# Optimization experiments

Measured on AMD Instinct MI355X. Metric: run time of the kernel, lower is better.

The kernel has to match this reference:

```python
import jax, jax.numpy as jnp
import numpy as np

N, D, E = 100000, 64, 1250000  # nodes, feature dim, total signed edges
H = D // 2                     # per-polarity hidden dim


def _mean_agg(x, src, dst, n):
    """Mean-aggregate messages x[src] at dst over n segments (gather->scatter)."""
    s = jax.ops.segment_sum(x[src], dst, num_segments=n)
    cnt = jax.ops.segment_sum(jnp.ones((src.shape[0], 1), x.dtype), dst, num_segments=n)
    return s / jnp.maximum(cnt, 1.0)


def _lin_w(k, fi, fo):
    b = 1.0 / np.sqrt(fi)
    return jax.random.uniform(k, (fi, fo), jnp.float32, -b, b)


def setup_inputs() -> dict:
    key = jax.random.key(0)
    ks = list(jax.random.split(key, 24))
    init_emb = jax.random.normal(ks[0], (N, D), dtype=jnp.float32)
    src = jax.random.randint(ks[1], (E,), 0, N)
    dst = jax.random.randint(ks[2], (E,), 0, N)
    sign = jnp.where(jax.random.uniform(ks[3], (E,)) < 0.5, 1, -1)
    edge_index_s = jnp.stack([src, dst, sign], axis=1)
    return dict(
        init_emb=init_emb,
        edge_index_s=edge_index_s,
        # conv1 (first_aggr=True): lin([mean_agg, x]) per polarity -> H
        Wp1=_lin_w(ks[4], 2 * D, H), bp1=jnp.zeros((H,), jnp.float32),
        Wn1=_lin_w(ks[5], 2 * D, H), bn1=jnp.zeros((H,), jnp.float32),
        # rest conv: lin([agg_pos, agg_neg, x_half]) per polarity -> H
        Wp2=_lin_w(ks[6], 3 * H, H), bp2=jnp.zeros((H,), jnp.float32),
        Wn2=_lin_w(ks[7], 3 * H, H), bn2=jnp.zeros((H,), jnp.float32),
        # final linear D->D
        Ww=_lin_w(ks[8], D, D), bw=jnp.zeros((D,), jnp.float32),
        # MLP readout: Linear+BN+ReLU, Linear+BN+ReLU, Linear->1 (inference mode)
        Wm1=_lin_w(ks[9], D, D), bm1=jnp.zeros((D,), jnp.float32),
        g1=jnp.ones((D,), jnp.float32), be1=jnp.zeros((D,), jnp.float32),
        rm1=jnp.zeros((D,), jnp.float32), rv1=jnp.ones((D,), jnp.float32),
        Wm2=_lin_w(ks[10], D, D), bm2=jnp.zeros((D,), jnp.float32),
        g2=jnp.ones((D,), jnp.float32), be2=jnp.zeros((D,), jnp.float32),
        rm2=jnp.zeros((D,), jnp.float32), rv2=jnp.ones((D,), jnp.float32),
        Wm3=_lin_w(ks[11], D, 1), bm3=jnp.zeros((1,), jnp.float32),
    )


def reference(init_emb, edge_index_s, Wp1, bp1, Wn1, bn1, Wp2, bp2, Wn2, bn2,
              Ww, bw, Wm1, bm1, g1, be1, rm1, rv1, Wm2, bm2, g2, be2, rm2, rv2,
              Wm3, bm3):
    # split signed edge list into pos / neg edge indices (eager boolean mask,
    # mirrors edge_index_s[edge_index_s[:,2]>0][:, :2].t())
    sign = edge_index_s[:, 2]
    pos = edge_index_s[sign > 0]
    neg = edge_index_s[sign < 0]
    ps, pd = pos[:, 0], pos[:, 1]
    ns, nd = neg[:, 0], neg[:, 1]

    x = init_emb
    # --- first signed conv (first_aggr=True) ---
    ap = _mean_agg(x, ps, pd, N)
    an = _mean_agg(x, ns, nd, N)
    hp = jnp.concatenate([ap, x], -1) @ Wp1 + bp1
    hn = jnp.concatenate([an, x], -1) @ Wn1 + bn1
    z = jnp.tanh(jnp.concatenate([hp, hn], -1))  # [N, D]

    # --- rest signed conv (balance-theory cross-polarity aggregation) ---
    xp, xn = z[:, :H], z[:, H:]
    hp = jnp.concatenate([_mean_agg(xp, ps, pd, N), _mean_agg(xn, ns, nd, N), xp], -1) @ Wp2 + bp2
    hn = jnp.concatenate([_mean_agg(xn, ps, pd, N), _mean_agg(xp, ns, nd, N), xn], -1) @ Wn2 + bn2
    z = jnp.tanh(jnp.concatenate([hp, hn], -1))  # [N, D]

    # --- final linear + tanh ---
    z = jnp.tanh(z @ Ww + bw)

    # --- MLP readout (inference: BN uses running stats, dropout disabled) ---
    def bn(h, g, b, rm, rv):
        return (h - rm) * jax.lax.rsqrt(rv + 1e-5) * g + b

    h = jax.nn.relu(bn(z @ Wm1 + bm1, g1, be1, rm1, rv1))
    h = jax.nn.relu(bn(h @ Wm2 + bm2, g2, be2, rm2, rv2))
    prob = jax.nn.sigmoid(h @ Wm3 + bm3)  # [N, 1]
    return z, prob
```

## Files before the change

kernel.cpp:

```cpp
#include <hip/hip_runtime.h>
#include <hip/hip_bf16.h>

#define CAP 32

typedef __attribute__((ext_vector_type(8))) short bf16x8;
typedef __attribute__((ext_vector_type(4))) float f32x4;

#define MFMA(a, b, c) __builtin_amdgcn_mfma_f32_16x16x32_bf16(a, b, c, 0, 0, 0)

__device__ __forceinline__ unsigned short bf16rn(float f) {
    unsigned u = __builtin_bit_cast(unsigned, f);
    u += 0x7fffu + ((u >> 16) & 1u);
    return (unsigned short)(u >> 16);
}

__device__ __forceinline__ float bf16lo(unsigned u) {
    return __builtin_bit_cast(float, u << 16);
}
__device__ __forceinline__ float bf16hi(unsigned u) {
    return __builtin_bit_cast(float, u & 0xffff0000u);
}
__device__ __forceinline__ unsigned pack2(float a, float b) {
    return (unsigned)bf16rn(a) | ((unsigned)bf16rn(b) << 16);
}

__device__ __forceinline__ bf16x8 packbf8(const float* p) {
    bf16x8 r;
    #pragma unroll
    for (int j = 0; j < 8; ++j) r[j] = (short)bf16rn(p[j]);
    return r;
}

__device__ __forceinline__ bf16x8 wfrag(const float* __restrict__ W, int NN,
                                        int kt, int ct, int q, int c) {
    const float* base = W + (kt * 32 + q * 8) * NN + ct * 16 + c;
    float t[8];
    #pragma unroll
    for (int j = 0; j < 8; ++j) t[j] = base[j * NN];
    return packbf8(t);
}

__device__ __forceinline__ bf16x8 afrag_bf16(const __hip_bfloat16* row, int cw, int q) {
    return *(const bf16x8*)((const short*)row + cw + q * 8);
}

__global__ __launch_bounds__(256) void pg_build_cast(
    const int* __restrict__ ei,
    int* __restrict__ plist, int* __restrict__ nlist,
    int* __restrict__ pcur, int* __restrict__ ncur, int E, int buildBlocks,
    const float* __restrict__ x, __hip_bfloat16* __restrict__ xb, int nx)
{
    int b = blockIdx.x;
    if (b >= buildBlocks) {
        int i = ((b - buildBlocks) * 256 + threadIdx.x) * 4;
        if (i < nx) {
            float4 v = *(const float4*)(x + i);
            ushort4 o;
            o.x = bf16rn(v.x); o.y = bf16rn(v.y);
            o.z = bf16rn(v.z); o.w = bf16rn(v.w);
            *(ushort4*)((unsigned short*)xb + i) = o;
        }
        return;
    }
    int e0 = (b * 256 + threadIdx.x) * 4;
    int s[4], d[4], sg[4];
    bool ok[4];
    #pragma unroll
    for (int k = 0; k < 4; ++k) {
        int e = e0 + k;
        ok[k] = (e < E);
        int ee = ok[k] ? e : 0;
        s[k]  = ei[3 * ee + 0];
        d[k]  = ei[3 * ee + 1];
        sg[k] = ei[3 * ee + 2];
    }
    int slot[4];
    int* dstl[4];
    #pragma unroll
    for (int k = 0; k < 4; ++k) {
        int* cur = (sg[k] > 0) ? pcur : ncur;
        dstl[k]  = ((sg[k] > 0) ? plist : nlist) + (size_t)d[k] * CAP;
        slot[k]  = ok[k] ? atomicAdd(cur + d[k], 1) : CAP;
    }
    #pragma unroll
    for (int k = 0; k < 4; ++k)
        if (slot[k] < CAP) dstl[k][slot[k]] = s[k];
}

__global__ __launch_bounds__(256, 6) void pg_gather(
    const __hip_bfloat16* __restrict__ src,
    const int* __restrict__ plist, const int* __restrict__ nlist,
    const int* __restrict__ pcur, const int* __restrict__ ncur,
    __hip_bfloat16* __restrict__ agg, int N)
{
    int tid = threadIdx.x;
    int w = tid >> 6, lane = tid & 63;
    int grp = lane >> 4;
    int q   = lane & 15;

    #pragma unroll 1
    for (int g = 0; g < 4; ++g) {
        int i0 = blockIdx.x * 64 + w * 16 + g * 4;
        int pd[4], nd[4], pde[4], nde[4], pl[4], nl[4];
        #pragma unroll
        for (int n = 0; n < 4; ++n) {
            int i = min(i0 + n, N - 1);
            pd[n] = __builtin_amdgcn_readfirstlane(pcur[i]);
            nd[n] = __builtin_amdgcn_readfirstlane(ncur[i]);
            pde[n] = min(pd[n], CAP);
            nde[n] = min(nd[n], CAP);
            pl[n] = plist[(size_t)i * CAP + (lane & 31)];
            nl[n] = nlist[(size_t)i * CAP + (lane & 31)];
        }
        int maxd = 0;
        #pragma unroll
        for (int n = 0; n < 4; ++n) maxd = max(maxd, max(pde[n], nde[n]));

        float ps[4][4], ns[4][4];
        #pragma unroll
        for (int n = 0; n < 4; ++n)
            #pragma unroll
            for (int r = 0; r < 4; ++r) { ps[n][r] = 0.f; ns[n][r] = 0.f; }

        #pragma unroll 1
        for (int e = 0; e < maxd; e += 4) {
            #pragma unroll
            for (int n = 0; n < 4; ++n) {
                int p0 = __builtin_amdgcn_readlane(pl[n], (e + 0) < pde[n] ? e + 0 : 0);
                int p1 = __builtin_amdgcn_readlane(pl[n], (e + 1) < pde[n] ? e + 1 : 0);
                int p2 = __builtin_amdgcn_readlane(pl[n], (e + 2) < pde[n] ? e + 2 : 0);
                int p3 = __builtin_amdgcn_readlane(pl[n], (e + 3) < pde[n] ? e + 3 : 0);
                int m0 = __builtin_amdgcn_readlane(nl[n], (e + 0) < nde[n] ? e + 0 : 0);
                int m1 = __builtin_amdgcn_readlane(nl[n], (e + 1) < nde[n] ? e + 1 : 0);
                int m2 = __builtin_amdgcn_readlane(nl[n], (e + 2) < nde[n] ? e + 2 : 0);
                int m3 = __builtin_amdgcn_readlane(nl[n], (e + 3) < nde[n] ? e + 3 : 0);
                unsigned sp = (unsigned)(grp == 0 ? p0 : grp == 1 ? p1 : grp == 2 ? p2 : p3);
                unsigned sn = (unsigned)(grp == 0 ? m0 : grp == 1 ? m1 : grp == 2 ? m2 : m3);
                sp = sp < (unsigned)N ? sp : 0u;
                sn = sn < (unsigned)N ? sn : 0u;
                uint2 pv = *((const uint2*)(src + ((size_t)sp << 6)) + q);
                uint2 nv = *((const uint2*)(src + ((size_t)sn << 6)) + q);
                float wp  = (e + grp < pde[n]) ? 1.f : 0.f;
                float wn_ = (e + grp < nde[n]) ? 1.f : 0.f;
                ps[n][0] = fmaf(wp, bf16lo(pv.x), ps[n][0]);
                ps[n][1] = fmaf(wp, bf16hi(pv.x), ps[n][1]);
                ps[n][2] = fmaf(wp, bf16lo(pv.y), ps[n][2]);
                ps[n][3] = fmaf(wp, bf16hi(pv.y), ps[n][3]);
                ns[n][0] = fmaf(wn_, bf16lo(nv.x), ns[n][0]);
                ns[n][1] = fmaf(wn_, bf16hi(nv.x), ns[n][1]);
                ns[n][2] = fmaf(wn_, bf16lo(nv.y), ns[n][2]);
                ns[n][3] = fmaf(wn_, bf16hi(nv.y), ns[n][3]);
            }
        }
        #pragma unroll
        for (int n = 0; n < 4; ++n) {
            #pragma unroll
            for (int r = 0; r < 4; ++r) {
                ps[n][r] += __shfl_xor(ps[n][r], 16);
                ps[n][r] += __shfl_xor(ps[n][r], 32);
                ns[n][r] += __shfl_xor(ns[n][r], 16);
                ns[n][r] += __shfl_xor(ns[n][r], 32);
            }
            int i = i0 + n;
            if (i < N) {
                float invp = 1.f / fmaxf((float)pd[n], 1.f);
                float invn = 1.f / fmaxf((float)nd[n], 1.f);
                uint2* arow = (uint2*)(agg + ((size_t)i << 7));
                if (grp == 0) {
                    uint2 ow;
                    ow.x = pack2(ps[n][0] * invp, ps[n][1] * invp);
                    ow.y = pack2(ps[n][2] * invp, ps[n][3] * invp);
                    arow[q] = ow;
                } else if (grp == 1) {
                    uint2 ow;
                    ow.x = pack2(ns[n][0] * invn, ns[n][1] * invn);
                    ow.y = pack2(ns[n][2] * invn, ns[n][3] * invn);
                    arow[16 + q] = ow;
                }
            }
        }
    }
}

__global__ __launch_bounds__(256, 3) void pg_gemm1(
    const __hip_bfloat16* __restrict__ xb, const __hip_bfloat16* __restrict__ agg,
    const float* __restrict__ Wp, const float* __restrict__ bp,
    const float* __restrict__ Wn, const float* __restrict__ bn,
    __hip_bfloat16* __restrict__ z1b, int N, int nwv)
{
    int tid = threadIdx.x;
    int w = tid >> 6, lane = tid & 63;
    int q = lane >> 4, c = lane & 15;

    bf16x8 B[2][4][2];
    #pragma unroll
    for (int kt = 0; kt < 4; ++kt)
        #pragma unroll
        for (int ct = 0; ct < 2; ++ct) {
            B[0][kt][ct] = wfrag(Wp, 32, kt, ct, q, c);
            B[1][kt][ct] = wfrag(Wn, 32, kt, ct, q, c);
        }
    float bias[2][2];
    #pragma unroll
    for (int ct = 0; ct < 2; ++ct) {
        bias[0][ct] = bp[ct * 16 + c];
        bias[1][ct] = bn[ct * 16 + c];
    }

    int ntiles = (N + 15) >> 4;
    #pragma unroll 1
    for (int t = blockIdx.x * 4 + w; t < ntiles; t += nwv) {
        int i = min(t * 16 + c, N - 1);
        const __hip_bfloat16* arow = agg + ((size_t)i << 7);
        const __hip_bfloat16* xrow = xb + ((size_t)i << 6);
        bf16x8 aA0 = afrag_bf16(arow, 0, q);
        bf16x8 aA1 = afrag_bf16(arow, 32, q);
        bf16x8 aA2 = afrag_bf16(arow, 64, q);
        bf16x8 aA3 = afrag_bf16(arow, 96, q);
        bf16x8 aX0 = afrag_bf16(xrow, 0, q);
        bf16x8 aX1 = afrag_bf16(xrow, 32, q);
        f32x4 acc[2][2];
        #pragma unroll
        for (int ct = 0; ct < 2; ++ct) {
            f32x4 a = {0.f, 0.f, 0.f, 0.f};
            a = MFMA(aA0, B[0][0][ct], a);
            a = MFMA(aA1, B[0][1][ct], a);
            a = MFMA(aX0, B[0][2][ct], a);
            a = MFMA(aX1, B[0][3][ct], a);
            acc[0][ct] = a;
            f32x4 b = {0.f, 0.f, 0.f, 0.f};
            b = MFMA(aA2, B[1][0][ct], b);
            b = MFMA(aA3, B[1][1][ct], b);
            b = MFMA(aX0, B[1][2][ct], b);
            b = MFMA(aX1, B[1][3][ct], b);
            acc[1][ct] = b;
        }
        #pragma unroll
        for (int h = 0; h < 2; ++h)
            #pragma unroll
            for (int ct = 0; ct < 2; ++ct)
                #pragma unroll
                for (int r = 0; r < 4; ++r) {
                    int row = t * 16 + q * 4 + r;
                    if (row < N)
                        z1b[(size_t)row * 64 + h * 32 + ct * 16 + c] =
                            __float2bfloat16(tanhf(acc[h][ct][r] + bias[h][ct]));
                }
    }
}

__global__ __launch_bounds__(256, 3) void pg_gemm2(
    const __hip_bfloat16* __restrict__ z1b, __hip_bfloat16* agg,
    const float* __restrict__ Wp2, const float* __restrict__ bp2,
    const float* __restrict__ Wn2, const float* __restrict__ bn2,
    int N, int nwv)
{
    int tid = threadIdx.x;
    int w = tid >> 6, lane = tid & 63;
    int q = lane >> 4, c = lane & 15;

    bf16x8 B[2][3][2];
    #pragma unroll
    for (int kt = 0; kt < 3; ++kt)
        #pragma unroll
        for (int ct = 0; ct < 2; ++ct) {
            B[0][kt][ct] = wfrag(Wp2, 32, kt, ct, q, c);
            B[1][kt][ct] = wfrag(Wn2, 32, kt, ct, q, c);
        }
    float bias[2][2];
    #pragma unroll
    for (int ct = 0; ct < 2; ++ct) {
        bias[0][ct] = bp2[ct * 16 + c];
        bias[1][ct] = bn2[ct * 16 + c];
    }

    int ntiles = (N + 15) >> 4;
    #pragma unroll 1
    for (int t = blockIdx.x * 4 + w; t < ntiles; t += nwv) {
        int i = min(t * 16 + c, N - 1);
        const __hip_bfloat16* arow = agg + ((size_t)i << 7);
        const __hip_bfloat16* zrow = z1b + ((size_t)i << 6);
        bf16x8 ap0 = afrag_bf16(arow, 0, q);
        bf16x8 ap1 = afrag_bf16(arow, 96, q);
        bf16x8 an0 = afrag_bf16(arow, 32, q);
        bf16x8 an1 = afrag_bf16(arow, 64, q);
        bf16x8 az0 = afrag_bf16(zrow, 0, q);
        bf16x8 az1 = afrag_bf16(zrow, 32, q);
        f32x4 acc[2][2];
        #pragma unroll
        for (int ct = 0; ct < 2; ++ct) {
            f32x4 a = {0.f, 0.f, 0.f, 0.f};
            a = MFMA(ap0, B[0][0][ct], a);
            a = MFMA(ap1, B[0][1][ct], a);
            a = MFMA(az0, B[0][2][ct], a);
            acc[0][ct] = a;
            f32x4 b = {0.f, 0.f, 0.f, 0.f};
            b = MFMA(an0, B[1][0][ct], b);
            b = MFMA(an1, B[1][1][ct], b);
            b = MFMA(az1, B[1][2][ct], b);
            acc[1][ct] = b;
        }
        #pragma unroll
        for (int h = 0; h < 2; ++h)
            #pragma unroll
            for (int ct = 0; ct < 2; ++ct)
                #pragma unroll
                for (int r = 0; r < 4; ++r) {
                    int row = t * 16 + q * 4 + r;
                    if (row < N)
                        agg[(size_t)row * 128 + h * 32 + ct * 16 + c] =
                            __float2bfloat16(tanhf(acc[h][ct][r] + bias[h][ct]));
                }
    }
}

__global__ __launch_bounds__(256, 2) void pg_mlp(
    float* out, const __hip_bfloat16* __restrict__ z2b,
    const float* __restrict__ Ww,  const float* __restrict__ bw,
    const float* __restrict__ Wm1, const float* __restrict__ bm1,
    const float* __restrict__ g1,  const float* __restrict__ be1,
    const float* __restrict__ rm1, const float* __restrict__ rv1,
    const float* __restrict__ Wm2, const float* __restrict__ bm2,
    const float* __restrict__ g2,  const float* __restrict__ be2,
    const float* __restrict__ rm2, const float* __restrict__ rv2,
    const float* __restrict__ Wm3, const float* __restrict__ bm3,
    int N, int nwv)
{
    __shared__ float xpos[4][16][68];
    int tid = threadIdx.x;
    int w = tid >> 6, lane = tid & 63;
    int q = lane >> 4, c = lane & 15;
    float (*lx)[68] = xpos[w];

    bf16x8 Bw[2][4], B1[2][4], B2[2][4];
    #pragma unroll
    for (int kt = 0; kt < 2; ++kt)
        #pragma unroll
        for (int ct = 0; ct < 4; ++ct) {
            Bw[kt][ct] = wfrag(Ww,  64, kt, ct, q, c);
            B1[kt][ct] = wfrag(Wm1, 64, kt, ct, q, c);
            B2[kt][ct] = wfrag(Wm2, 64, kt, ct, q, c);
        }
    float bwv[4], s1[4], o1[4], s2[4], o2[4], w3[4];
    #pragma unroll
    for (int ct = 0; ct < 4; ++ct) {
        int cc = ct * 16 + c;
        bwv[ct] = bw[cc];
        float a = g1[cc] * rsqrtf(rv1[cc] + 1e-5f);
        s1[ct] = a; o1[ct] = (bm1[cc] - rm1[cc]) * a + be1[cc];
        float b = g2[cc] * rsqrtf(rv2[cc] + 1e-5f);
        s2[ct] = b; o2[ct] = (bm2[cc] - rm2[cc]) * b + be2[cc];
        w3[ct] = Wm3[cc];
    }
    float b3 = bm3[0];

    int ntiles = (N + 15) >> 4;
    #pragma unroll 1
    for (int t = blockIdx.x * 4 + w; t < ntiles; t += nwv) {
        int i = min(t * 16 + c, N - 1);
        const __hip_bfloat16* zrow = z2b + ((size_t)i << 7);
        bf16x8 a0 = afrag_bf16(zrow, 0, q);
        bf16x8 a1 = afrag_bf16(zrow, 32, q);
        f32x4 acc[4];

        #pragma unroll
        for (int ct = 0; ct < 4; ++ct) {
            f32x4 a = {0.f, 0.f, 0.f, 0.f};
            a = MFMA(a0, Bw[0][ct], a);
            a = MFMA(a1, Bw[1][ct], a);
            acc[ct] = a;
        }
        #pragma unroll
        for (int ct = 0; ct < 4; ++ct)
            #pragma unroll
            for (int r = 0; r < 4; ++r) {
                int row = t * 16 + q * 4 + r;
                float v = tanhf(acc[ct][r] + bwv[ct]);
                if (row < N) out[(size_t)row * 64 + ct * 16 + c] = v;
                lx[q * 4 + r][ct * 16 + c] = v;
            }
        {
            const float* pr = &lx[c][0];
            float tb[8];
            *(float4*)tb       = *(const float4*)(pr + q * 8);
            *(float4*)(tb + 4) = *(const float4*)(pr + q * 8 + 4);
            a0 = packbf8(tb);
            *(float4*)tb       = *(const float4*)(pr + 32 + q * 8);
            *(float4*)(tb + 4) = *(const float4*)(pr + 32 + q * 8 + 4);
            a1 = packbf8(tb);
        }

        #pragma unroll
        for (int ct = 0; ct < 4; ++ct) {
            f32x4 a = {0.f, 0.f, 0.f, 0.f};
            a = MFMA(a0, B1[0][ct], a);
            a = MFMA(a1, B1[1][ct], a);
            acc[ct] = a;
        }
        #pragma unroll
        for (int ct = 0; ct < 4; ++ct)
            #pragma unroll
            for (int r = 0; r < 4; ++r)
                lx[q * 4 + r][ct * 16 + c] = fmaxf(acc[ct][r] * s1[ct] + o1[ct], 0.f);
        {
            const float* pr = &lx[c][0];
            float tb[8];
            *(float4*)tb       = *(const float4*)(pr + q * 8);
            *(float4*)(tb + 4) = *(const float4*)(pr + q * 8 + 4);
            a0 = packbf8(tb);
            *(float4*)tb       = *(const float4*)(pr + 32 + q * 8);
            *(float4*)(tb + 4) = *(const float4*)(pr + 32 + q * 8 + 4);
            a1 = packbf8(tb);
        }

        #pragma unroll
        for (int ct = 0; ct < 4; ++ct) {
            f32x4 a = {0.f, 0.f, 0.f, 0.f};
            a = MFMA(a0, B2[0][ct], a);
            a = MFMA(a1, B2[1][ct], a);
            acc[ct] = a;
        }
        float tr[4];
        #pragma unroll
        for (int r = 0; r < 4; ++r) {
            float hs = 0.f;
            #pragma unroll
            for (int ct = 0; ct < 4; ++ct) {
                float h2 = fmaxf(acc[ct][r] * s2[ct] + o2[ct], 0.f);
                hs = fmaf(h2, w3[ct], hs);
            }
            tr[r] = hs;
        }
        #pragma unroll
        for (int m = 1; m < 16; m <<= 1)
            #pragma unroll
            for (int r = 0; r < 4; ++r) tr[r] += __shfl_xor(tr[r], m, 16);
        if (c == 0) {
            #pragma unroll
            for (int r = 0; r < 4; ++r) {
                int row = t * 16 + q * 4 + r;
                if (row < N)
                    out[(size_t)N * 64 + row] = 1.f / (1.f + expf(-(tr[r] + b3)));
            }
        }
    }
}

extern "C" void kernel_launch(void* const* d_in, const int* in_sizes, int n_in,
                              void* d_out, int out_size, void* d_ws, size_t ws_size,
                              hipStream_t stream) {
    const float* x   = (const float*)d_in[0];
    const int*   ei  = (const int*)  d_in[1];
    const float* Wp1 = (const float*)d_in[2];
    const float* bp1 = (const float*)d_in[3];
    const float* Wn1 = (const float*)d_in[4];
    const float* bn1 = (const float*)d_in[5];
    const float* Wp2 = (const float*)d_in[6];
    const float* bp2 = (const float*)d_in[7];
    const float* Wn2 = (const float*)d_in[8];
    const float* bn2 = (const float*)d_in[9];
    const float* Ww  = (const float*)d_in[10];
    const float* bw  = (const float*)d_in[11];
    const float* Wm1 = (const float*)d_in[12];
    const float* bm1 = (const float*)d_in[13];
    const float* g1  = (const float*)d_in[14];
    const float* be1 = (const float*)d_in[15];
    const float* rm1 = (const float*)d_in[16];
    const float* rv1 = (const float*)d_in[17];
    const float* Wm2 = (const float*)d_in[18];
    const float* bm2 = (const float*)d_in[19];
    const float* g2  = (const float*)d_in[20];
    const float* be2 = (const float*)d_in[21];
    const float* rm2 = (const float*)d_in[22];
    const float* rv2 = (const float*)d_in[23];
    const float* Wm3 = (const float*)d_in[24];
    const float* bm3 = (const float*)d_in[25];
    float* out = (float*)d_out;

    int N = in_sizes[0] / 64;
    int E = in_sizes[1] / 3;

    int* plist = (int*)d_ws;
    int* nlist = plist + (size_t)N * CAP;
    int* pcur  = nlist + (size_t)N * CAP;
    int* ncur  = pcur + N;
    __hip_bfloat16* agg = (__hip_bfloat16*)(ncur + N);

    __hip_bfloat16* z1b = (__hip_bfloat16*)out;
    __hip_bfloat16* xb  = (__hip_bfloat16*)((char*)d_out + (size_t)N * 128);

    hipMemsetAsync(pcur, 0, 2 * (size_t)N * sizeof(int), stream);

    int buildBlocks = (E + 1023) / 1024;
    int castBlocks  = (N * 64 / 4 + 255) / 256;
    pg_build_cast<<<buildBlocks + castBlocks, 256, 0, stream>>>(
        ei, plist, nlist, pcur, ncur, E, buildBlocks, x, xb, N * 64);

    int nb = (N + 63) / 64;
    const int gb = 512, nwv = gb * 4;
    pg_gather<<<nb, 256, 0, stream>>>(xb, plist, nlist, pcur, ncur, agg, N);
    pg_gemm1<<<gb, 256, 0, stream>>>(xb, agg, Wp1, bp1, Wn1, bn1, z1b, N, nwv);
    pg_gather<<<nb, 256, 0, stream>>>(z1b, plist, nlist, pcur, ncur, agg, N);
    pg_gemm2<<<gb, 256, 0, stream>>>(z1b, agg, Wp2, bp2, Wn2, bn2, N, nwv);
    pg_mlp<<<gb, 256, 0, stream>>>(out, agg, Ww, bw,
                                   Wm1, bm1, g1, be1, rm1, rv1,
                                   Wm2, bm2, g2, be2, rm2, rv2,
                                   Wm3, bm3, N, nwv);
}
```

Baseline: 258.2 us.

## Fuse neighbor gather with per-layer MFMA GEMM via LDS staging

Merges each gather kernel with the following linear+tanh kernel. The mean aggregates for 16 nodes per wave are staged in LDS and fed straight into the MFMA fragments, so the bf16 agg buffer is no longer written to and re-read from global memory, and two launches are dropped. The gather also now predicates each neighbor load on validity instead of loading a dummy row and multiplying by zero. In exchange, weights are reloaded per block and occupancy is set to 4 waves per SIMD with added LDS use.

```diff
diff --git a/kernel.cpp b/kernel.cpp
--- a/kernel.cpp
+++ b/kernel.cpp
@@ -13,7 +13,6 @@
     u += 0x7fffu + ((u >> 16) & 1u);
     return (unsigned short)(u >> 16);
 }
-
 __device__ __forceinline__ float bf16lo(unsigned u) {
     return __builtin_bit_cast(float, u << 16);
 }
@@ -23,7 +22,6 @@
 __device__ __forceinline__ unsigned pack2(float a, float b) {
     return (unsigned)bf16rn(a) | ((unsigned)bf16rn(b) << 16);
 }
-
 __device__ __forceinline__ bf16x8 packbf8(const float* p) {
     bf16x8 r;
     #pragma unroll
@@ -42,6 +40,14 @@
 
 __device__ __forceinline__ bf16x8 afrag_bf16(const __hip_bfloat16* row, int cw, int q) {
     return *(const bf16x8*)((const short*)row + cw + q * 8);
+}
+
+__device__ __forceinline__ bf16x8 lfrag(const short* lrow, int cw, int q8) {
+    const uint2* p = (const uint2*)(lrow + cw + q8 * 8);
+    uint2 lo = p[0], hi = p[1];
+    uint4 u;
+    u.x = lo.x; u.y = lo.y; u.z = hi.x; u.w = hi.y;
+    return __builtin_bit_cast(bf16x8, u);
 }
 
 __global__ __launch_bounds__(256) void pg_build_cast(
@@ -87,118 +93,110 @@
         if (slot[k] < CAP) dstl[k][slot[k]] = s[k];
 }
 
-__global__ __launch_bounds__(256, 6) void pg_gather(
-    const __hip_bfloat16* __restrict__ src,
+
+#define GATHER_16NODES(SRC)                                                     \
+    for (int g = 0; g < 4; ++g) {                                               \
+        int i0 = base + g * 4;                                                  \
+        int pd[4], nd[4], pde[4], nde[4], pl[4], nl[4];                         \
+        _Pragma("unroll")                                                       \
+        for (int n = 0; n < 4; ++n) {                                           \
+            int i = min(i0 + n, N - 1);                                         \
+            pd[n] = __builtin_amdgcn_readfirstlane(pcur[i]);                    \
+            nd[n] = __builtin_amdgcn_readfirstlane(ncur[i]);                    \
+            pde[n] = min(pd[n], CAP);                                           \
+            nde[n] = min(nd[n], CAP);                                           \
+            pl[n] = plist[(size_t)i * CAP + (lane & 31)];                       \
+            nl[n] = nlist[(size_t)i * CAP + (lane & 31)];                       \
+        }                                                                       \
+        int maxd = 0;                                                           \
+        _Pragma("unroll")                                                       \
+        for (int n = 0; n < 4; ++n) maxd = max(maxd, max(pde[n], nde[n]));      \
+        float ps[4][4], ns[4][4];                                               \
+        _Pragma("unroll")                                                       \
+        for (int n = 0; n < 4; ++n)                                             \
+            _Pragma("unroll")                                                   \
+            for (int r = 0; r < 4; ++r) { ps[n][r] = 0.f; ns[n][r] = 0.f; }     \
+        _Pragma("unroll 1")                                                     \
+        for (int e = 0; e < maxd; e += 4) {                                     \
+            _Pragma("unroll")                                                   \
+            for (int n = 0; n < 4; ++n) {                                       \
+                int p0 = __builtin_amdgcn_readlane(pl[n], (e+0) < pde[n] ? e+0 : 0); \
+                int p1 = __builtin_amdgcn_readlane(pl[n], (e+1) < pde[n] ? e+1 : 0); \
+                int p2 = __builtin_amdgcn_readlane(pl[n], (e+2) < pde[n] ? e+2 : 0); \
+                int p3 = __builtin_amdgcn_readlane(pl[n], (e+3) < pde[n] ? e+3 : 0); \
+                int m0 = __builtin_amdgcn_readlane(nl[n], (e+0) < nde[n] ? e+0 : 0); \
+                int m1 = __builtin_amdgcn_readlane(nl[n], (e+1) < nde[n] ? e+1 : 0); \
+                int m2 = __builtin_amdgcn_readlane(nl[n], (e+2) < nde[n] ? e+2 : 0); \
+                int m3 = __builtin_amdgcn_readlane(nl[n], (e+3) < nde[n] ? e+3 : 0); \
+                unsigned sp = (unsigned)(grp == 0 ? p0 : grp == 1 ? p1 : grp == 2 ? p2 : p3); \
+                unsigned sn = (unsigned)(grp == 0 ? m0 : grp == 1 ? m1 : grp == 2 ? m2 : m3); \
+                if (e + grp < pde[n]) {                                         \
+                    sp = sp < (unsigned)N ? sp : 0u;                            \
+                    uint2 pv = *((const uint2*)((SRC) + ((size_t)sp << 6)) + q);\
+                    ps[n][0] += bf16lo(pv.x); ps[n][1] += bf16hi(pv.x);         \
+                    ps[n][2] += bf16lo(pv.y); ps[n][3] += bf16hi(pv.y);         \
+                }                                                               \
+                if (e + grp < nde[n]) {                                         \
+                    sn = sn < (unsigned)N ? sn : 0u;                            \
+                    uint2 nv = *((const uint2*)((SRC) + ((size_t)sn << 6)) + q);\
+                    ns[n][0] += bf16lo(nv.x); ns[n][1] += bf16hi(nv.x);         \
+                    ns[n][2] += bf16lo(nv.y); ns[n][3] += bf16hi(nv.y);         \
+                }                                                               \
+            }                                                                   \
+        }                                                                       \
+        _Pragma("unroll")                                                       \
+        for (int n = 0; n < 4; ++n) {                                           \
+            _Pragma("unroll")                                                   \
+            for (int r = 0; r < 4; ++r) {                                       \
+                ps[n][r] += __shfl_xor(ps[n][r], 16);                           \
+                ps[n][r] += __shfl_xor(ps[n][r], 32);                           \
+                ns[n][r] += __shfl_xor(ns[n][r], 16);                           \
+                ns[n][r] += __shfl_xor(ns[n][r], 32);                           \
+            }                                                                   \
+            float invp = 1.f / fmaxf((float)pd[n], 1.f);                        \
+            float invn = 1.f / fmaxf((float)nd[n], 1.f);                        \
+            short* lrow = &lds[(g * 4 + n) * 132];                              \
+            if (grp == 0) {                                                     \
+                uint2 ow;                                                       \
+                ow.x = pack2(ps[n][0] * invp, ps[n][1] * invp);                 \
+                ow.y = pack2(ps[n][2] * invp, ps[n][3] * invp);                 \
+                *(uint2*)(lrow + 4 * q) = ow;                                   \
+            } else if (grp == 1) {                                              \
+                uint2 ow;                                                       \
+                ow.x = pack2(ns[n][0] * invn, ns[n][1] * invn);                 \
+                ow.y = pack2(ns[n][2] * invn, ns[n][3] * invn);                 \
+                *(uint2*)(lrow + 64 + 4 * q) = ow;                              \
+            }                                                                   \
+        }                                                                       \
+    }
+
+__global__ __launch_bounds__(256, 4) void pg_layer1(
+    const __hip_bfloat16* __restrict__ xb,
     const int* __restrict__ plist, const int* __restrict__ nlist,
     const int* __restrict__ pcur, const int* __restrict__ ncur,
-    __hip_bfloat16* __restrict__ agg, int N)
+    const float* __restrict__ Wp, const float* __restrict__ bp,
+    const float* __restrict__ Wn, const float* __restrict__ bn,
+    __hip_bfloat16* __restrict__ z1b, int N)
 {
+    __shared__ short smem[4][16 * 132];
     int tid = threadIdx.x;
     int w = tid >> 6, lane = tid & 63;
-    int grp = lane >> 4;
-    int q   = lane & 15;
-
-    #pragma unroll 1
-    for (int g = 0; g < 4; ++g) {
-        int i0 = blockIdx.x * 64 + w * 16 + g * 4;
-        int pd[4], nd[4], pde[4], nde[4], pl[4], nl[4];
-        #pragma unroll
-        for (int n = 0; n < 4; ++n) {
-            int i = min(i0 + n, N - 1);
-            pd[n] = __builtin_amdgcn_readfirstlane(pcur[i]);
-            nd[n] = __builtin_amdgcn_readfirstlane(ncur[i]);
-            pde[n] = min(pd[n], CAP);
-            nde[n] = min(nd[n], CAP);
-            pl[n] = plist[(size_t)i * CAP + (lane & 31)];
-            nl[n] = nlist[(size_t)i * CAP + (lane & 31)];
-        }
-        int maxd = 0;
-        #pragma unroll
-        for (int n = 0; n < 4; ++n) maxd = max(maxd, max(pde[n], nde[n]));
-
-        float ps[4][4], ns[4][4];
-        #pragma unroll
-        for (int n = 0; n < 4; ++n)
-            #pragma unroll
-            for (int r = 0; r < 4; ++r) { ps[n][r] = 0.f; ns[n][r] = 0.f; }
-
-        #pragma unroll 1
-        for (int e = 0; e < maxd; e += 4) {
-            #pragma unroll
-            for (int n = 0; n < 4; ++n) {
-                int p0 = __builtin_amdgcn_readlane(pl[n], (e + 0) < pde[n] ? e + 0 : 0);
-                int p1 = __builtin_amdgcn_readlane(pl[n], (e + 1) < pde[n] ? e + 1 : 0);
-                int p2 = __builtin_amdgcn_readlane(pl[n], (e + 2) < pde[n] ? e + 2 : 0);
-                int p3 = __builtin_amdgcn_readlane(pl[n], (e + 3) < pde[n] ? e + 3 : 0);
-                int m0 = __builtin_amdgcn_readlane(nl[n], (e + 0) < nde[n] ? e + 0 : 0);
-                int m1 = __builtin_amdgcn_readlane(nl[n], (e + 1) < nde[n] ? e + 1 : 0);
-                int m2 = __builtin_amdgcn_readlane(nl[n], (e + 2) < nde[n] ? e + 2 : 0);
-                int m3 = __builtin_amdgcn_readlane(nl[n], (e + 3) < nde[n] ? e + 3 : 0);
-                unsigned sp = (unsigned)(grp == 0 ? p0 : grp == 1 ? p1 : grp == 2 ? p2 : p3);
-                unsigned sn = (unsigned)(grp == 0 ? m0 : grp == 1 ? m1 : grp == 2 ? m2 : m3);
-                sp = sp < (unsigned)N ? sp : 0u;
-                sn = sn < (unsigned)N ? sn : 0u;
-                uint2 pv = *((const uint2*)(src + ((size_t)sp << 6)) + q);
-                uint2 nv = *((const uint2*)(src + ((size_t)sn << 6)) + q);
-                float wp  = (e + grp < pde[n]) ? 1.f : 0.f;
-                float wn_ = (e + grp < nde[n]) ? 1.f : 0.f;
-                ps[n][0] = fmaf(wp, bf16lo(pv.x), ps[n][0]);
-                ps[n][1] = fmaf(wp, bf16hi(pv.x), ps[n][1]);
-                ps[n][2] = fmaf(wp, bf16lo(pv.y), ps[n][2]);
-                ps[n][3] = fmaf(wp, bf16hi(pv.y), ps[n][3]);
-                ns[n][0] = fmaf(wn_, bf16lo(nv.x), ns[n][0]);
-                ns[n][1] = fmaf(wn_, bf16hi(nv.x), ns[n][1]);
-                ns[n][2] = fmaf(wn_, bf16lo(nv.y), ns[n][2]);
-                ns[n][3] = fmaf(wn_, bf16hi(nv.y), ns[n][3]);
-            }
-        }
-        #pragma unroll
-        for (int n = 0; n < 4; ++n) {
-            #pragma unroll
-            for (int r = 0; r < 4; ++r) {
-                ps[n][r] += __shfl_xor(ps[n][r], 16);
-                ps[n][r] += __shfl_xor(ps[n][r], 32);
-                ns[n][r] += __shfl_xor(ns[n][r], 16);
-                ns[n][r] += __shfl_xor(ns[n][r], 32);
-            }
-            int i = i0 + n;
-            if (i < N) {
-                float invp = 1.f / fmaxf((float)pd[n], 1.f);
-                float invn = 1.f / fmaxf((float)nd[n], 1.f);
-                uint2* arow = (uint2*)(agg + ((size_t)i << 7));
-                if (grp == 0) {
-                    uint2 ow;
-                    ow.x = pack2(ps[n][0] * invp, ps[n][1] * invp);
-                    ow.y = pack2(ps[n][2] * invp, ps[n][3] * invp);
-                    arow[q] = ow;
-                } else if (grp == 1) {
-                    uint2 ow;
-                    ow.x = pack2(ns[n][0] * invn, ns[n][1] * invn);
-                    ow.y = pack2(ns[n][2] * invn, ns[n][3] * invn);
-                    arow[16 + q] = ow;
-                }
-            }
-        }
-    }
-}
-
-__global__ __launch_bounds__(256, 3) void pg_gemm1(
-    const __hip_bfloat16* __restrict__ xb, const __hip_bfloat16* __restrict__ agg,
-    const float* __restrict__ Wp, const float* __restrict__ bp,
-    const float* __restrict__ Wn, const float* __restrict__ bn,
-    __hip_bfloat16* __restrict__ z1b, int N, int nwv)
-{
-    int tid = threadIdx.x;
-    int w = tid >> 6, lane = tid & 63;
-    int q = lane >> 4, c = lane & 15;
-
+    int grp = lane >> 4, q = lane & 15;
+    short* lds = smem[w];
+    int base = blockIdx.x * 64 + w * 16;
+
+    GATHER_16NODES(xb)
+
+    __builtin_amdgcn_sched_barrier(0);
+
+    int q8 = lane >> 4, c = lane & 15;
     bf16x8 B[2][4][2];
     #pragma unroll
     for (int kt = 0; kt < 4; ++kt)
         #pragma unroll
         for (int ct = 0; ct < 2; ++ct) {
-            B[0][kt][ct] = wfrag(Wp, 32, kt, ct, q, c);
-            B[1][kt][ct] = wfrag(Wn, 32, kt, ct, q, c);
+            B[0][kt][ct] = wfrag(Wp, 32, kt, ct, q8, c);
+            B[1][kt][ct] = wfrag(Wn, 32, kt, ct, q8, c);
         }
     float bias[2][2];
     #pragma unroll
@@ -206,66 +204,71 @@
         bias[0][ct] = bp[ct * 16 + c];
         bias[1][ct] = bn[ct * 16 + c];
     }
-
-    int ntiles = (N + 15) >> 4;
-    #pragma unroll 1
-    for (int t = blockIdx.x * 4 + w; t < ntiles; t += nwv) {
-        int i = min(t * 16 + c, N - 1);
-        const __hip_bfloat16* arow = agg + ((size_t)i << 7);
-        const __hip_bfloat16* xrow = xb + ((size_t)i << 6);
-        bf16x8 aA0 = afrag_bf16(arow, 0, q);
-        bf16x8 aA1 = afrag_bf16(arow, 32, q);
-        bf16x8 aA2 = afrag_bf16(arow, 64, q);
-        bf16x8 aA3 = afrag_bf16(arow, 96, q);
-        bf16x8 aX0 = afrag_bf16(xrow, 0, q);
-        bf16x8 aX1 = afrag_bf16(xrow, 32, q);
-        f32x4 acc[2][2];
-        #pragma unroll
-        for (int ct = 0; ct < 2; ++ct) {
-            f32x4 a = {0.f, 0.f, 0.f, 0.f};
-            a = MFMA(aA0, B[0][0][ct], a);
-            a = MFMA(aA1, B[0][1][ct], a);
-            a = MFMA(aX0, B[0][2][ct], a);
-            a = MFMA(aX1, B[0][3][ct], a);
-            acc[0][ct] = a;
-            f32x4 b = {0.f, 0.f, 0.f, 0.f};
-            b = MFMA(aA2, B[1][0][ct], b);
-            b = MFMA(aA3, B[1][1][ct], b);
-            b = MFMA(aX0, B[1][2][ct], b);
-            b = MFMA(aX1, B[1][3][ct], b);
-            acc[1][ct] = b;
-        }
-        #pragma unroll
-        for (int h = 0; h < 2; ++h)
-            #pragma unroll
-            for (int ct = 0; ct < 2; ++ct)
-                #pragma unroll
-                for (int r = 0; r < 4; ++r) {
-                    int row = t * 16 + q * 4 + r;
-                    if (row < N)
-                        z1b[(size_t)row * 64 + h * 32 + ct * 16 + c] =
-                            __float2bfloat16(tanhf(acc[h][ct][r] + bias[h][ct]));
-                }
-    }
-}
-
-__global__ __launch_bounds__(256, 3) void pg_gemm2(
-    const __hip_bfloat16* __restrict__ z1b, __hip_bfloat16* agg,
+    int i = min(base + c, N - 1);
+    const __hip_bfloat16* xrow = xb + ((size_t)i << 6);
+    const short* lrow = &lds[c * 132];
+    bf16x8 aA0 = lfrag(lrow, 0, q8);
+    bf16x8 aA1 = lfrag(lrow, 32, q8);
+    bf16x8 aA2 = lfrag(lrow, 64, q8);
+    bf16x8 aA3 = lfrag(lrow, 96, q8);
+    bf16x8 aX0 = afrag_bf16(xrow, 0, q8);
+    bf16x8 aX1 = afrag_bf16(xrow, 32, q8);
+    f32x4 acc[2][2];
+    #pragma unroll
+    for (int ct = 0; ct < 2; ++ct) {
+        f32x4 a = {0.f, 0.f, 0.f, 0.f};
+        a = MFMA(aA0, B[0][0][ct], a);
+        a = MFMA(aA1, B[0][1][ct], a);
+        a = MFMA(aX0, B[0][2][ct], a);
+        a = MFMA(aX1, B[0][3][ct], a);
+        acc[0][ct] = a;
+        f32x4 b = {0.f, 0.f, 0.f, 0.f};
+        b = MFMA(aA2, B[1][0][ct], b);
+        b = MFMA(aA3, B[1][1][ct], b);
+        b = MFMA(aX0, B[1][2][ct], b);
+        b = MFMA(aX1, B[1][3][ct], b);
+        acc[1][ct] = b;
+    }
+    #pragma unroll
+    for (int h = 0; h < 2; ++h)
+        #pragma unroll
+        for (int ct = 0; ct < 2; ++ct)
+            #pragma unroll
+            for (int r = 0; r < 4; ++r) {
+                int row = base + q8 * 4 + r;
+                if (row < N)
+                    z1b[(size_t)row * 64 + h * 32 + ct * 16 + c] =
+                        __float2bfloat16(tanhf(acc[h][ct][r] + bias[h][ct]));
+            }
+}
+
+__global__ __launch_bounds__(256, 4) void pg_layer2(
+    const __hip_bfloat16* __restrict__ z1b,
+    const int* __restrict__ plist, const int* __restrict__ nlist,
+    const int* __restrict__ pcur, const int* __restrict__ ncur,
     const float* __restrict__ Wp2, const float* __restrict__ bp2,
     const float* __restrict__ Wn2, const float* __restrict__ bn2,
-    int N, int nwv)
+    __hip_bfloat16* __restrict__ z2b, int N)
 {
+    __shared__ short smem[4][16 * 132];
     int tid = threadIdx.x;
     int w = tid >> 6, lane = tid & 63;
-    int q = lane >> 4, c = lane & 15;
-
+    int grp = lane >> 4, q = lane & 15;
+    short* lds = smem[w];
+    int base = blockIdx.x * 64 + w * 16;
+
+    GATHER_16NODES(z1b)
+
+    __builtin_amdgcn_sched_barrier(0);
+
+    int q8 = lane >> 4, c = lane & 15;
     bf16x8 B[2][3][2];
     #pragma unroll
     for (int kt = 0; kt < 3; ++kt)
         #pragma unroll
         for (int ct = 0; ct < 2; ++ct) {
-            B[0][kt][ct] = wfrag(Wp2, 32, kt, ct, q, c);
-            B[1][kt][ct] = wfrag(Wn2, 32, kt, ct, q, c);
+            B[0][kt][ct] = wfrag(Wp2, 32, kt, ct, q8, c);
+            B[1][kt][ct] = wfrag(Wn2, 32, kt, ct, q8, c);
         }
     float bias[2][2];
     #pragma unroll
@@ -273,45 +276,40 @@
         bias[0][ct] = bp2[ct * 16 + c];
         bias[1][ct] = bn2[ct * 16 + c];
     }
-
-    int ntiles = (N + 15) >> 4;
-    #pragma unroll 1
-    for (int t = blockIdx.x * 4 + w; t < ntiles; t += nwv) {
-        int i = min(t * 16 + c, N - 1);
-        const __hip_bfloat16* arow = agg + ((size_t)i << 7);
-        const __hip_bfloat16* zrow = z1b + ((size_t)i << 6);
-        bf16x8 ap0 = afrag_bf16(arow, 0, q);
-        bf16x8 ap1 = afrag_bf16(arow, 96, q);
-        bf16x8 an0 = afrag_bf16(arow, 32, q);
-        bf16x8 an1 = afrag_bf16(arow, 64, q);
-        bf16x8 az0 = afrag_bf16(zrow, 0, q);
-        bf16x8 az1 = afrag_bf16(zrow, 32, q);
-        f32x4 acc[2][2];
-        #pragma unroll
-        for (int ct = 0; ct < 2; ++ct) {
-            f32x4 a = {0.f, 0.f, 0.f, 0.f};
-            a = MFMA(ap0, B[0][0][ct], a);
-            a = MFMA(ap1, B[0][1][ct], a);
-            a = MFMA(az0, B[0][2][ct], a);
-            acc[0][ct] = a;
-            f32x4 b = {0.f, 0.f, 0.f, 0.f};
-            b = MFMA(an0, B[1][0][ct], b);
-            b = MFMA(an1, B[1][1][ct], b);
-            b = MFMA(az1, B[1][2][ct], b);
-            acc[1][ct] = b;
-        }
-        #pragma unroll
-        for (int h = 0; h < 2; ++h)
-            #pragma unroll
-            for (int ct = 0; ct < 2; ++ct)
-                #pragma unroll
-                for (int r = 0; r < 4; ++r) {
-                    int row = t * 16 + q * 4 + r;
-                    if (row < N)
-                        agg[(size_t)row * 128 + h * 32 + ct * 16 + c] =
-                            __float2bfloat16(tanhf(acc[h][ct][r] + bias[h][ct]));
-                }
-    }
+    int i = min(base + c, N - 1);
+    const __hip_bfloat16* zrow = z1b + ((size_t)i << 6);
+    const short* lrow = &lds[c * 132];
+    bf16x8 ap0 = lfrag(lrow, 0, q8);
+    bf16x8 ap1 = lfrag(lrow, 96, q8);
+    bf16x8 an0 = lfrag(lrow, 32, q8);
+    bf16x8 an1 = lfrag(lrow, 64, q8);
+    bf16x8 az0 = afrag_bf16(zrow, 0, q8);
+    bf16x8 az1 = afrag_bf16(zrow, 32, q8);
+    f32x4 acc[2][2];
+    #pragma unroll
+    for (int ct = 0; ct < 2; ++ct) {
+        f32x4 a = {0.f, 0.f, 0.f, 0.f};
+        a = MFMA(ap0, B[0][0][ct], a);
+        a = MFMA(ap1, B[0][1][ct], a);
+        a = MFMA(az0, B[0][2][ct], a);
+        acc[0][ct] = a;
+        f32x4 b = {0.f, 0.f, 0.f, 0.f};
+        b = MFMA(an0, B[1][0][ct], b);
+        b = MFMA(an1, B[1][1][ct], b);
+        b = MFMA(az1, B[1][2][ct], b);
+        acc[1][ct] = b;
+    }
+    #pragma unroll
+    for (int h = 0; h < 2; ++h)
+        #pragma unroll
+        for (int ct = 0; ct < 2; ++ct)
+            #pragma unroll
+            for (int r = 0; r < 4; ++r) {
+                int row = base + q8 * 4 + r;
+                if (row < N)
+                    z2b[(size_t)row * 128 + h * 32 + ct * 16 + c] =
+                        __float2bfloat16(tanhf(acc[h][ct][r] + bias[h][ct]));
+            }
 }
 
 __global__ __launch_bounds__(256, 2) void pg_mlp(
@@ -484,7 +482,7 @@
     int* nlist = plist + (size_t)N * CAP;
     int* pcur  = nlist + (size_t)N * CAP;
     int* ncur  = pcur + N;
-    __hip_bfloat16* agg = (__hip_bfloat16*)(ncur + N);
+    __hip_bfloat16* z2b = (__hip_bfloat16*)(ncur + N);
 
     __hip_bfloat16* z1b = (__hip_bfloat16*)out;
     __hip_bfloat16* xb  = (__hip_bfloat16*)((char*)d_out + (size_t)N * 128);
@@ -497,12 +495,12 @@
         ei, plist, nlist, pcur, ncur, E, buildBlocks, x, xb, N * 64);
 
     int nb = (N + 63) / 64;
+    pg_layer1<<<nb, 256, 0, stream>>>(xb, plist, nlist, pcur, ncur,
+                                      Wp1, bp1, Wn1, bn1, z1b, N);
+    pg_layer2<<<nb, 256, 0, stream>>>(z1b, plist, nlist, pcur, ncur,
+                                      Wp2, bp2, Wn2, bn2, z2b, N);
     const int gb = 512, nwv = gb * 4;
-    pg_gather<<<nb, 256, 0, stream>>>(xb, plist, nlist, pcur, ncur, agg, N);
-    pg_gemm1<<<gb, 256, 0, stream>>>(xb, agg, Wp1, bp1, Wn1, bn1, z1b, N, nwv);
-    pg_gather<<<nb, 256, 0, stream>>>(z1b, plist, nlist, pcur, ncur, agg, N);
-    pg_gemm2<<<gb, 256, 0, stream>>>(z1b, agg, Wp2, bp2, Wn2, bn2, N, nwv);
-    pg_mlp<<<gb, 256, 0, stream>>>(out, agg, Ww, bw,
+    pg_mlp<<<gb, 256, 0, stream>>>(out, z2b, Ww, bw,
                                    Wm1, bm1, g1, be1, rm1, rv1,
                                    Wm2, bm2, g2, be2, rm2, rv2,
                                    Wm3, bm3, N, nwv);
```

Result: slower. 267.6 us (+3.6%).
